# Performance work log

Measured on AMD Instinct MI355X. Metric: run time of the kernel, lower is better.

The kernel has to match this reference:

```python
import jax, jax.numpy as jnp
import numpy as np

DECAY = 0.99
EPS = 1e-05


def setup_inputs() -> dict:
    key = jax.random.key(0)
    k1, k2, k3 = jax.random.split(key, 3)
    N, K, D = 131072, 1024, 64
    return {
        "z": jax.random.normal(k1, (N, D), dtype=jnp.float32),
        "embeddings": jax.random.normal(k2, (K, D), dtype=jnp.float32),
        "cluster_size": jnp.ones((K,), dtype=jnp.float32),
        "ema_embed_sum": jax.random.normal(k3, (K, D), dtype=jnp.float32),
    }


def reference(z, embeddings, cluster_size, ema_embed_sum):
    # z: [N, D]; embeddings/ema_embed_sum: [K, D]; cluster_size: [K]
    N, D = z.shape
    K = embeddings.shape[0]

    # squared pairwise distances via the ||a||^2 - 2ab + ||b||^2 expansion
    d = (
        jnp.sum(z * z, axis=-1, keepdims=True)
        - 2.0 * (z @ embeddings.T)
        + jnp.sum(embeddings * embeddings, axis=-1)
    )  # [N, K]
    encoding_indices = jnp.argmin(d, axis=1)  # [N]
    z_q = embeddings[encoding_indices]  # [N, D]

    # EMA codebook update (training mode; one_hot.sum(0) == counts, one_hot.T @ z == segment_sum)
    counts = jax.ops.segment_sum(jnp.ones((N,), z.dtype), encoding_indices, num_segments=K)
    new_cluster_size = cluster_size * DECAY + (1.0 - DECAY) * counts
    embed_sum = jax.ops.segment_sum(z, encoding_indices, num_segments=K)  # [K, D]
    new_ema_embed_sum = ema_embed_sum * DECAY + (1.0 - DECAY) * embed_sum
    n = jnp.sum(new_cluster_size)
    cs = (new_cluster_size + EPS) / (n + K * EPS) * n
    new_embeddings = new_ema_embed_sum / cs[:, None]

    commitment_loss = jnp.mean((z - z_q) ** 2)
    z_q_st = z + jax.lax.stop_gradient(z_q - z)  # value == z_q
    return (z_q_st, commitment_loss, encoding_indices, new_embeddings, new_cluster_size, new_ema_embed_sum)
```

## Files before the change

kernel.cpp:

```cpp
#include <hip/hip_runtime.h>

#define N_PTS 131072
#define K_CODES 1024
#define DIM 64
#define DECAYF 0.99f
#define OMDF 0.01f
#define EPSF 1e-5f

#define OUT_ZQ      0
#define OUT_LOSS    8388608
#define OUT_IDX     8388609
#define OUT_NEWEMB  8519681
#define OUT_NEWCS   8585217
#define OUT_NEWEMA  8586241

#define WS_C8       0
#define WS_ACNT     8192
#define WS_LOSS     8208
#define WS_EMBSUM   8224
#define WS_ZERO_END 73760
#define WS_ENORM    73760
#define WS_CUR8     74784
#define WS_CS       82976
#define WS_AMBIG    84000
#define WS_ORDER    215072
#define WS_E2       346144

typedef __attribute__((ext_vector_type(8))) short bf16x8;
typedef __attribute__((ext_vector_type(4))) float f32x4;

static __device__ inline short f2bf(float f) {
    unsigned u = __float_as_uint(f);
    unsigned r = (u + 0x7fffu + ((u >> 16) & 1u)) >> 16;
    return (short)r;
}
static __device__ inline float bf2f(short h) {
    return __uint_as_float(((unsigned)(unsigned short)h) << 16);
}

__global__ __launch_bounds__(256) void econv_kernel(const float* __restrict__ E,
                                                    short* __restrict__ E2,
                                                    float* __restrict__ enorm) {
    int k = blockIdx.x * 256 + threadIdx.x;
    const float* ep = E + (size_t)k * DIM;
    short* o = E2 + (size_t)k * 128;
    float s = 0.f;
#pragma unroll
    for (int d = 0; d < 64; ++d) {
        float f = ep[d];
        s += f * f;
        float m = -2.f * f;
        short h = f2bf(m);
        o[d] = h;
        o[64 + d] = f2bf(m - bf2f(h));
    }
    enorm[k] = s;
}

__global__ __launch_bounds__(256) void argmin_mfma(const float* __restrict__ z,
                                                   const short* __restrict__ E2,
                                                   const float* __restrict__ enorm,
                                                   float* __restrict__ out_idx_f,
                                                   float* __restrict__ counts8,
                                                   int* __restrict__ ambig_cnt,
                                                   int* __restrict__ ambig,
                                                   float* __restrict__ loss_ws) {
    int tid = threadIdx.x;
    int w = tid >> 6, lane = tid & 63;
    int c = lane & 15, q = lane >> 4;
    int mbase = blockIdx.x * 256 + w * 64;

    bf16x8 a[4][4];
    float znorm_t[4];
#pragma unroll
    for (int t = 0; t < 4; ++t) {
        const float* zp = z + (size_t)(mbase + t * 16 + c) * DIM;
        const float4* z4a = (const float4*)(zp + q * 8);
        const float4* z4b = (const float4*)(zp + 32 + q * 8);
        float f[16];
        float4 v0 = z4a[0], v1 = z4a[1], v2 = z4b[0], v3 = z4b[1];
        f[0]=v0.x; f[1]=v0.y; f[2]=v0.z; f[3]=v0.w;
        f[4]=v1.x; f[5]=v1.y; f[6]=v1.z; f[7]=v1.w;
        f[8]=v2.x; f[9]=v2.y; f[10]=v2.z; f[11]=v2.w;
        f[12]=v3.x; f[13]=v3.y; f[14]=v3.z; f[15]=v3.w;
        float zn = 0.f;
#pragma unroll
        for (int j = 0; j < 16; ++j) zn += f[j] * f[j];
#pragma unroll
        for (int off = 16; off < 64; off <<= 1) zn += __shfl_xor(zn, off);
        znorm_t[t] = zn;
#pragma unroll
        for (int j = 0; j < 8; ++j) {
            short h0 = f2bf(f[j]);
            a[t][0][j] = h0;
            a[t][2][j] = f2bf(f[j] - bf2f(h0));
            short h1 = f2bf(f[8 + j]);
            a[t][1][j] = h1;
            a[t][3][j] = f2bf(f[8 + j] - bf2f(h1));
        }
    }

    float s1[16], s2[16];
#pragma unroll
    for (int idx = 0; idx < 16; ++idx) { s1[idx] = INFINITY; s2[idx] = INFINITY; }

    unsigned vcode = (unsigned)c;
    for (int tile = 0; tile < 64; ++tile) {
        const bf16x8* bp = (const bf16x8*)E2 + ((size_t)(tile * 16 + c) * 16) + q;
        bf16x8 bh0 = bp[0], bh1 = bp[4], bl0 = bp[8], bl1 = bp[12];
        float en = enorm[tile * 16 + c];
#pragma unroll
        for (int t = 0; t < 4; ++t) {
            f32x4 acc = {en, en, en, en};
            acc = __builtin_amdgcn_mfma_f32_16x16x32_bf16(a[t][0], bl0, acc, 0, 0, 0);
            acc = __builtin_amdgcn_mfma_f32_16x16x32_bf16(a[t][1], bl1, acc, 0, 0, 0);
            acc = __builtin_amdgcn_mfma_f32_16x16x32_bf16(a[t][2], bh0, acc, 0, 0, 0);
            acc = __builtin_amdgcn_mfma_f32_16x16x32_bf16(a[t][3], bh1, acc, 0, 0, 0);
            acc = __builtin_amdgcn_mfma_f32_16x16x32_bf16(a[t][0], bh0, acc, 0, 0, 0);
            acc = __builtin_amdgcn_mfma_f32_16x16x32_bf16(a[t][1], bh1, acc, 0, 0, 0);
#pragma unroll
            for (int i = 0; i < 4; ++i) {
                float sp = __uint_as_float(
                    (__float_as_uint(acc[i]) & 0xFFFFFC00u) | vcode);
                int idx = t * 4 + i;
                float ns2 = __builtin_amdgcn_fmed3f(s1[idx], s2[idx], sp);
                s1[idx] = fminf(s1[idx], sp);
                s2[idx] = ns2;
            }
        }
        vcode += 16;
    }

#pragma unroll
    for (int off = 1; off < 16; off <<= 1) {
#pragma unroll
        for (int idx = 0; idx < 16; ++idx) {
            float os1 = __shfl_xor(s1[idx], off);
            float os2 = __shfl_xor(s2[idx], off);
            float ns1 = fminf(s1[idx], os1);
            s2[idx] = fminf(fmaxf(s1[idx], os1), fminf(s2[idx], os2));
            s1[idx] = ns1;
        }
    }

    float znr[16];
#pragma unroll
    for (int t = 0; t < 4; ++t)
#pragma unroll
        for (int i = 0; i < 4; ++i)
            znr[t * 4 + i] = __shfl(znorm_t[t], (q << 4) | (q * 4 + i), 64);

    __shared__ float lred[16];
    float lsum = 0.f;
    if (c == 0) {
#pragma unroll
        for (int idx = 0; idx < 16; ++idx) {
            int t = idx >> 2, i = idx & 3;
            int row = mbase + t * 16 + q * 4 + i;
            unsigned b1 = __float_as_uint(s1[idx]);
            int code = (int)(b1 & 1023u);
            out_idx_f[row] = (float)code;
            float s1v = __uint_as_float(b1 & 0xFFFFFC00u);
            float gap = s2[idx] - s1[idx];
            float tau = 0.008f + 8e-4f * (fabsf(s1[idx]) + fabsf(s2[idx]));
            if (gap >= tau) {
                atomicAdd(&counts8[(((unsigned)row >> 8) & 7) * K_CODES + code], 1.0f);
                lsum += znr[idx] + s1v;
            } else {
                int p = atomicAdd(ambig_cnt, 1);
                ambig[p] = row;
            }
        }
        lred[w * 4 + q] = lsum;
    }
    __syncthreads();
    if (tid == 0) {
        float tot = 0.f;
#pragma unroll
        for (int i = 0; i < 16; ++i) tot += lred[i];
        atomicAdd(loss_ws, tot);
    }
}

__global__ __launch_bounds__(256) void rescue_kernel(const float* __restrict__ z,
                                                     const float* __restrict__ E,
                                                     const float* __restrict__ enorm,
                                                     const int* __restrict__ ambig_cnt,
                                                     const int* __restrict__ ambig,
                                                     float* __restrict__ out_idx_f,
                                                     float* __restrict__ counts8,
                                                     float* __restrict__ loss_ws) {
    int lane = threadIdx.x & 63;
    int wave = (blockIdx.x * 256 + threadIdx.x) >> 6;
    int nw = gridDim.x * 4;
    int cnt = *ambig_cnt;
    for (int a = 2 * wave; a < cnt; a += 2 * nw) {
        int row0 = ambig[a];
        bool two = (a + 1) < cnt;
        int row1 = two ? ambig[a + 1] : row0;
        const float4* zp0 = (const float4*)(z + (size_t)row0 * DIM);
        const float4* zp1 = (const float4*)(z + (size_t)row1 * DIM);
        float4 zr0[16], zr1[16];
        float zn0 = 0.f, zn1 = 0.f;
#pragma unroll
        for (int i = 0; i < 16; ++i) {
            float4 u = zp0[i], v = zp1[i];
            zr0[i] = u; zr1[i] = v;
            zn0 += u.x * u.x + u.y * u.y + u.z * u.z + u.w * u.w;
            zn1 += v.x * v.x + v.y * v.y + v.z * v.z + v.w * v.w;
        }
        float best0 = INFINITY, best1 = INFINITY;
        int bi0 = 0, bi1 = 0;
        for (int j = 0; j < 16; ++j) {
            int code = j * 64 + lane;
            const float4* ep = (const float4*)(E + (size_t)code * DIM);
            float a0 = 0.f, a1 = 0.f, a2 = 0.f, a3 = 0.f;
            float c0 = 0.f, c1 = 0.f, c2 = 0.f, c3 = 0.f;
#pragma unroll
            for (int i = 0; i < 16; ++i) {
                float4 ev = ep[i];
                a0 += zr0[i].x * ev.x; a1 += zr0[i].y * ev.y;
                a2 += zr0[i].z * ev.z; a3 += zr0[i].w * ev.w;
                c0 += zr1[i].x * ev.x; c1 += zr1[i].y * ev.y;
                c2 += zr1[i].z * ev.z; c3 += zr1[i].w * ev.w;
            }
            float en = enorm[code];
            float s0 = en - 2.f * ((a0 + a1) + (a2 + a3));
            float s1 = en - 2.f * ((c0 + c1) + (c2 + c3));
            if (s0 < best0) { best0 = s0; bi0 = code; }
            if (s1 < best1) { best1 = s1; bi1 = code; }
        }
#pragma unroll
        for (int off = 1; off < 64; off <<= 1) {
            float ob = __shfl_xor(best0, off);
            int oi = __shfl_xor(bi0, off);
            if (ob < best0 || (ob == best0 && oi < bi0)) { best0 = ob; bi0 = oi; }
            float ob1 = __shfl_xor(best1, off);
            int oi1 = __shfl_xor(bi1, off);
            if (ob1 < best1 || (ob1 == best1 && oi1 < bi1)) { best1 = ob1; bi1 = oi1; }
        }
        if (lane == 0) {
            out_idx_f[row0] = (float)bi0;
            atomicAdd(&counts8[(((unsigned)row0 >> 8) & 7) * K_CODES + bi0], 1.0f);
            float ladd = zn0 + best0;
            if (two) {
                out_idx_f[row1] = (float)bi1;
                atomicAdd(&counts8[(((unsigned)row1 >> 8) & 7) * K_CODES + bi1], 1.0f);
                ladd += zn1 + best1;
            }
            atomicAdd(loss_ws, ladd);
        }
    }
}

__global__ __launch_bounds__(256) void zq_write_kernel(const float* __restrict__ E,
                                                       const float* __restrict__ idx_f,
                                                       float* __restrict__ zq) {
    __shared__ int s_k[256];
    int tid = threadIdx.x;
    int rbase = blockIdx.x * 256;
    s_k[tid] = (int)idx_f[rbase + tid];
    __syncthreads();
    size_t ebase = (size_t)rbase * DIM;
#pragma unroll 4
    for (int it = 0; it < 64; ++it) {
        int le = it * 256 + tid;
        int rl = le >> 6, d = le & 63;
        zq[ebase + le] = E[(size_t)s_k[rl] * DIM + d];
    }
}

__global__ __launch_bounds__(1024) void scan_kernel(const float* __restrict__ cluster_size,
                                                    const float* __restrict__ counts8,
                                                    float* __restrict__ ncs_out,
                                                    float* __restrict__ cs_ws,
                                                    int* __restrict__ cursor8) {
    int k = threadIdx.x;
    int lane = k & 63, wv = k >> 6;
    float c8[8];
    float cnt = 0.f;
#pragma unroll
    for (int s = 0; s < 8; ++s) { c8[s] = counts8[s * K_CODES + k]; cnt += c8[s]; }
    float ncs = cluster_size[k] * DECAYF + OMDF * cnt;
    ncs_out[k] = ncs;

    int v = (int)cnt;
    int vs = v;
#pragma unroll
    for (int off = 1; off < 64; off <<= 1) {
        int o = __shfl_up(vs, off, 64);
        if (lane >= off) vs += o;
    }
    float fs = ncs;
#pragma unroll
    for (int off = 1; off < 64; off <<= 1) fs += __shfl_xor(fs, off);

    __shared__ int wtot[16];
    __shared__ float ftot[16];
    __shared__ float nsh;
    if (lane == 63) wtot[wv] = vs;
    if (lane == 0) ftot[wv] = fs;
    __syncthreads();
    if (k == 0) {
        int run = 0; float fn = 0.f;
#pragma unroll
        for (int i = 0; i < 16; ++i) {
            int t = wtot[i]; wtot[i] = run; run += t;
            fn += ftot[i];
        }
        nsh = fn;
    }
    __syncthreads();
    float n = nsh;
    cs_ws[k] = (ncs + EPSF) / (n + (float)K_CODES * EPSF) * n;

    int excl = vs - v + wtot[wv];
    int run = excl;
#pragma unroll
    for (int s = 0; s < 8; ++s) { cursor8[s * K_CODES + k] = run; run += (int)c8[s]; }
}

__global__ __launch_bounds__(256) void scatter_kernel(const float* __restrict__ idx_f,
                                                      int* __restrict__ cursor8,
                                                      int* __restrict__ order) {
    int row = blockIdx.x * 256 + threadIdx.x;
    int k = (int)idx_f[row];
    int shard = ((unsigned)row >> 8) & 7;
    int p = atomicAdd(&cursor8[shard * K_CODES + k], 1);
    order[p] = (k << 17) | row;
}

__global__ __launch_bounds__(256) void segsum_kernel(const float* __restrict__ z,
                                                     const int* __restrict__ order,
                                                     float* __restrict__ embsum) {
    int lane = threadIdx.x & 63;
    int w = threadIdx.x >> 6;
    int wave = blockIdx.x * 4 + w;
    int base = wave * 64;

    int my = order[base + lane];

    int cur = __shfl(my, 0, 64) >> 17;
    float sum = 0.f;
#pragma unroll 8
    for (int i = 0; i < 64; ++i) {
        int p = __shfl(my, i, 64);
        int row = p & 0x1FFFF;
        int code = p >> 17;
        float v = z[(size_t)row * DIM + lane];
        if (code != cur) {
            atomicAdd(&embsum[(size_t)cur * DIM + lane], sum);
            sum = 0.f;
            cur = code;
        }
        sum += v;
    }
    atomicAdd(&embsum[(size_t)cur * DIM + lane], sum);
}

__global__ __launch_bounds__(256) void ema2_kernel(const float* __restrict__ ema,
                                                   const float* __restrict__ embsum,
                                                   const float* __restrict__ cs_ws,
                                                   const float* __restrict__ loss_ws,
                                                   float* __restrict__ newema_out,
                                                   float* __restrict__ newemb_out,
                                                   float* __restrict__ loss_out) {
    int i = blockIdx.x * 256 + threadIdx.x;
    float nes = ema[i] * DECAYF + OMDF * embsum[i];
    newema_out[i] = nes;
    newemb_out[i] = nes / cs_ws[i >> 6];
    if (i == 0)
        loss_out[0] = loss_ws[0] * (1.0f / ((float)N_PTS * (float)DIM));
}

extern "C" void kernel_launch(void* const* d_in, const int* in_sizes, int n_in,
                              void* d_out, int out_size, void* d_ws, size_t ws_size,
                              hipStream_t stream) {
    const float* z            = (const float*)d_in[0];
    const float* E            = (const float*)d_in[1];
    const float* cluster_size = (const float*)d_in[2];
    const float* ema          = (const float*)d_in[3];
    float* out = (float*)d_out;
    float* ws  = (float*)d_ws;

    hipMemsetAsync(ws, 0, (size_t)WS_ZERO_END * sizeof(float), stream);

    econv_kernel<<<4, 256, 0, stream>>>(E, (short*)(ws + WS_E2), ws + WS_ENORM);

    argmin_mfma<<<N_PTS / 256, 256, 0, stream>>>(z, (const short*)(ws + WS_E2),
                                                 ws + WS_ENORM,
                                                 out + OUT_IDX,
                                                 ws + WS_C8,
                                                 (int*)(ws + WS_ACNT),
                                                 (int*)(ws + WS_AMBIG),
                                                 ws + WS_LOSS);

    rescue_kernel<<<512, 256, 0, stream>>>(z, E, ws + WS_ENORM,
                                           (const int*)(ws + WS_ACNT),
                                           (const int*)(ws + WS_AMBIG),
                                           out + OUT_IDX,
                                           ws + WS_C8,
                                           ws + WS_LOSS);

    zq_write_kernel<<<N_PTS / 256, 256, 0, stream>>>(E, out + OUT_IDX,
                                                     out + OUT_ZQ);

    scan_kernel<<<1, 1024, 0, stream>>>(cluster_size, ws + WS_C8,
                                        out + OUT_NEWCS, ws + WS_CS,
                                        (int*)(ws + WS_CUR8));

    scatter_kernel<<<N_PTS / 256, 256, 0, stream>>>(out + OUT_IDX,
                                                    (int*)(ws + WS_CUR8),
                                                    (int*)(ws + WS_ORDER));

    segsum_kernel<<<N_PTS / 256, 256, 0, stream>>>(z,
                                                   (const int*)(ws + WS_ORDER),
                                                   ws + WS_EMBSUM);

    ema2_kernel<<<K_CODES * DIM / 256, 256, 0, stream>>>(ema, ws + WS_EMBSUM,
                                                         ws + WS_CS,
                                                         ws + WS_LOSS,
                                                         out + OUT_NEWEMA,
                                                         out + OUT_NEWEMB,
                                                         out + OUT_LOSS);
}
```

Baseline: 249.0 us.

## Fuse z_q gather into argmin and rescue, shrink argmin tile, fold memset

The separate z_q gather kernel is removed. The argmin kernel now writes z_q rows for confidently assigned points, and the rescue kernel writes them for ambiguous points. The argmin kernel processes 16 rows per wave instead of 64 and launches four times as many blocks with an occupancy hint, trading reuse of each loaded E2 tile for lower register pressure and more waves in flight. The workspace memset is folded into extra blocks of the codebook-conversion kernel, which removes one launch.

```diff
diff --git a/kernel.cpp b/kernel.cpp
--- a/kernel.cpp
+++ b/kernel.cpp
@@ -40,7 +40,14 @@
 
 __global__ __launch_bounds__(256) void econv_kernel(const float* __restrict__ E,
                                                     short* __restrict__ E2,
-                                                    float* __restrict__ enorm) {
+                                                    float* __restrict__ enorm,
+                                                    float* __restrict__ ws0) {
+    if (blockIdx.x >= 4) {
+        for (int i = (blockIdx.x - 4) * 256 + threadIdx.x; i < WS_ZERO_END;
+             i += 32 * 256)
+            ws0[i] = 0.f;
+        return;
+    }
     int k = blockIdx.x * 256 + threadIdx.x;
     const float* ep = E + (size_t)k * DIM;
     short* o = E2 + (size_t)k * 128;
@@ -57,121 +64,119 @@
     enorm[k] = s;
 }
 
-__global__ __launch_bounds__(256) void argmin_mfma(const float* __restrict__ z,
-                                                   const short* __restrict__ E2,
-                                                   const float* __restrict__ enorm,
-                                                   float* __restrict__ out_idx_f,
-                                                   float* __restrict__ counts8,
-                                                   int* __restrict__ ambig_cnt,
-                                                   int* __restrict__ ambig,
-                                                   float* __restrict__ loss_ws) {
+__global__ __launch_bounds__(256, 6) void argmin_mfma(const float* __restrict__ z,
+                                                      const short* __restrict__ E2,
+                                                      const float* __restrict__ enorm,
+                                                      const float* __restrict__ E,
+                                                      float* __restrict__ out_idx_f,
+                                                      float* __restrict__ counts8,
+                                                      int* __restrict__ ambig_cnt,
+                                                      int* __restrict__ ambig,
+                                                      float* __restrict__ loss_ws,
+                                                      float* __restrict__ zq) {
     int tid = threadIdx.x;
     int w = tid >> 6, lane = tid & 63;
     int c = lane & 15, q = lane >> 4;
-    int mbase = blockIdx.x * 256 + w * 64;
-
-    bf16x8 a[4][4];
-    float znorm_t[4];
-#pragma unroll
-    for (int t = 0; t < 4; ++t) {
-        const float* zp = z + (size_t)(mbase + t * 16 + c) * DIM;
-        const float4* z4a = (const float4*)(zp + q * 8);
-        const float4* z4b = (const float4*)(zp + 32 + q * 8);
+    int mbase = blockIdx.x * 64 + w * 16;
+
+    bf16x8 a[4];
+    float zn;
+    {
+        const float* zp = z + (size_t)(mbase + c) * DIM;
+        float4 v0 = *(const float4*)(zp + q * 8);
+        float4 v1 = *(const float4*)(zp + q * 8 + 4);
+        float4 v2 = *(const float4*)(zp + 32 + q * 8);
+        float4 v3 = *(const float4*)(zp + 32 + q * 8 + 4);
         float f[16];
-        float4 v0 = z4a[0], v1 = z4a[1], v2 = z4b[0], v3 = z4b[1];
         f[0]=v0.x; f[1]=v0.y; f[2]=v0.z; f[3]=v0.w;
         f[4]=v1.x; f[5]=v1.y; f[6]=v1.z; f[7]=v1.w;
         f[8]=v2.x; f[9]=v2.y; f[10]=v2.z; f[11]=v2.w;
         f[12]=v3.x; f[13]=v3.y; f[14]=v3.z; f[15]=v3.w;
-        float zn = 0.f;
+        zn = 0.f;
 #pragma unroll
         for (int j = 0; j < 16; ++j) zn += f[j] * f[j];
-#pragma unroll
-        for (int off = 16; off < 64; off <<= 1) zn += __shfl_xor(zn, off);
-        znorm_t[t] = zn;
+        zn += __shfl_xor(zn, 16);
+        zn += __shfl_xor(zn, 32);
 #pragma unroll
         for (int j = 0; j < 8; ++j) {
             short h0 = f2bf(f[j]);
-            a[t][0][j] = h0;
-            a[t][2][j] = f2bf(f[j] - bf2f(h0));
+            a[0][j] = h0;
+            a[2][j] = f2bf(f[j] - bf2f(h0));
             short h1 = f2bf(f[8 + j]);
-            a[t][1][j] = h1;
-            a[t][3][j] = f2bf(f[8 + j] - bf2f(h1));
-        }
-    }
-
-    float s1[16], s2[16];
-#pragma unroll
-    for (int idx = 0; idx < 16; ++idx) { s1[idx] = INFINITY; s2[idx] = INFINITY; }
+            a[1][j] = h1;
+            a[3][j] = f2bf(f[8 + j] - bf2f(h1));
+        }
+    }
+
+    float s1[4] = {INFINITY, INFINITY, INFINITY, INFINITY};
+    float s2[4] = {INFINITY, INFINITY, INFINITY, INFINITY};
 
     unsigned vcode = (unsigned)c;
     for (int tile = 0; tile < 64; ++tile) {
         const bf16x8* bp = (const bf16x8*)E2 + ((size_t)(tile * 16 + c) * 16) + q;
         bf16x8 bh0 = bp[0], bh1 = bp[4], bl0 = bp[8], bl1 = bp[12];
         float en = enorm[tile * 16 + c];
-#pragma unroll
-        for (int t = 0; t < 4; ++t) {
-            f32x4 acc = {en, en, en, en};
-            acc = __builtin_amdgcn_mfma_f32_16x16x32_bf16(a[t][0], bl0, acc, 0, 0, 0);
-            acc = __builtin_amdgcn_mfma_f32_16x16x32_bf16(a[t][1], bl1, acc, 0, 0, 0);
-            acc = __builtin_amdgcn_mfma_f32_16x16x32_bf16(a[t][2], bh0, acc, 0, 0, 0);
-            acc = __builtin_amdgcn_mfma_f32_16x16x32_bf16(a[t][3], bh1, acc, 0, 0, 0);
-            acc = __builtin_amdgcn_mfma_f32_16x16x32_bf16(a[t][0], bh0, acc, 0, 0, 0);
-            acc = __builtin_amdgcn_mfma_f32_16x16x32_bf16(a[t][1], bh1, acc, 0, 0, 0);
+        f32x4 acc = {en, en, en, en};
+        acc = __builtin_amdgcn_mfma_f32_16x16x32_bf16(a[0], bl0, acc, 0, 0, 0);
+        acc = __builtin_amdgcn_mfma_f32_16x16x32_bf16(a[1], bl1, acc, 0, 0, 0);
+        acc = __builtin_amdgcn_mfma_f32_16x16x32_bf16(a[2], bh0, acc, 0, 0, 0);
+        acc = __builtin_amdgcn_mfma_f32_16x16x32_bf16(a[3], bh1, acc, 0, 0, 0);
+        acc = __builtin_amdgcn_mfma_f32_16x16x32_bf16(a[0], bh0, acc, 0, 0, 0);
+        acc = __builtin_amdgcn_mfma_f32_16x16x32_bf16(a[1], bh1, acc, 0, 0, 0);
+#pragma unroll
+        for (int i = 0; i < 4; ++i) {
+            float sp = __uint_as_float(
+                (__float_as_uint(acc[i]) & 0xFFFFFC00u) | vcode);
+            float ns2 = __builtin_amdgcn_fmed3f(s1[i], s2[i], sp);
+            s1[i] = fminf(s1[i], sp);
+            s2[i] = ns2;
+        }
+        vcode += 16;
+    }
+
+#pragma unroll
+    for (int off = 1; off < 16; off <<= 1) {
+#pragma unroll
+        for (int i = 0; i < 4; ++i) {
+            float os1 = __shfl_xor(s1[i], off);
+            float os2 = __shfl_xor(s2[i], off);
+            float ns1 = fminf(s1[i], os1);
+            s2[i] = fminf(fmaxf(s1[i], os1), fminf(s2[i], os2));
+            s1[i] = ns1;
+        }
+    }
+
+    float znr[4];
+#pragma unroll
+    for (int i = 0; i < 4; ++i) znr[i] = __shfl(zn, q * 4 + i);
+
+    __shared__ float lred[16];
+    int code_s[4], flag_s[4];
+    {
+        float lsum = 0.f;
+        if (c == 0) {
 #pragma unroll
             for (int i = 0; i < 4; ++i) {
-                float sp = __uint_as_float(
-                    (__float_as_uint(acc[i]) & 0xFFFFFC00u) | vcode);
-                int idx = t * 4 + i;
-                float ns2 = __builtin_amdgcn_fmed3f(s1[idx], s2[idx], sp);
-                s1[idx] = fminf(s1[idx], sp);
-                s2[idx] = ns2;
+                int row = mbase + q * 4 + i;
+                unsigned b1 = __float_as_uint(s1[i]);
+                int code = (int)(b1 & 1023u);
+                code_s[i] = code;
+                out_idx_f[row] = (float)code;
+                float s1v = __uint_as_float(b1 & 0xFFFFFC00u);
+                float gap = s2[i] - s1[i];
+                float tau = 0.008f + 8e-4f * (fabsf(s1[i]) + fabsf(s2[i]));
+                if (gap >= tau) {
+                    flag_s[i] = 1;
+                    atomicAdd(&counts8[(((unsigned)row >> 8) & 7) * K_CODES + code], 1.0f);
+                    lsum += znr[i] + s1v;
+                } else {
+                    flag_s[i] = 0;
+                    int p = atomicAdd(ambig_cnt, 1);
+                    ambig[p] = row;
+                }
             }
-        }
-        vcode += 16;
-    }
-
-#pragma unroll
-    for (int off = 1; off < 16; off <<= 1) {
-#pragma unroll
-        for (int idx = 0; idx < 16; ++idx) {
-            float os1 = __shfl_xor(s1[idx], off);
-            float os2 = __shfl_xor(s2[idx], off);
-            float ns1 = fminf(s1[idx], os1);
-            s2[idx] = fminf(fmaxf(s1[idx], os1), fminf(s2[idx], os2));
-            s1[idx] = ns1;
-        }
-    }
-
-    float znr[16];
-#pragma unroll
-    for (int t = 0; t < 4; ++t)
-#pragma unroll
-        for (int i = 0; i < 4; ++i)
-            znr[t * 4 + i] = __shfl(znorm_t[t], (q << 4) | (q * 4 + i), 64);
-
-    __shared__ float lred[16];
-    float lsum = 0.f;
-    if (c == 0) {
-#pragma unroll
-        for (int idx = 0; idx < 16; ++idx) {
-            int t = idx >> 2, i = idx & 3;
-            int row = mbase + t * 16 + q * 4 + i;
-            unsigned b1 = __float_as_uint(s1[idx]);
-            int code = (int)(b1 & 1023u);
-            out_idx_f[row] = (float)code;
-            float s1v = __uint_as_float(b1 & 0xFFFFFC00u);
-            float gap = s2[idx] - s1[idx];
-            float tau = 0.008f + 8e-4f * (fabsf(s1[idx]) + fabsf(s2[idx]));
-            if (gap >= tau) {
-                atomicAdd(&counts8[(((unsigned)row >> 8) & 7) * K_CODES + code], 1.0f);
-                lsum += znr[idx] + s1v;
-            } else {
-                int p = atomicAdd(ambig_cnt, 1);
-                ambig[p] = row;
-            }
-        }
-        lred[w * 4 + q] = lsum;
+            lred[w * 4 + q] = lsum;
+        }
     }
     __syncthreads();
     if (tid == 0) {
@@ -179,6 +184,15 @@
 #pragma unroll
         for (int i = 0; i < 16; ++i) tot += lred[i];
         atomicAdd(loss_ws, tot);
+    }
+
+#pragma unroll
+    for (int r = 0; r < 16; ++r) {
+        int holder = (r >> 2) << 4;
+        int code = __shfl(code_s[r & 3], holder);
+        int fl   = __shfl(flag_s[r & 3], holder);
+        if (fl)
+            zq[(size_t)(mbase + r) * DIM + lane] = E[(size_t)code * DIM + lane];
     }
 }
 
@@ -189,7 +203,8 @@
                                                      const int* __restrict__ ambig,
                                                      float* __restrict__ out_idx_f,
                                                      float* __restrict__ counts8,
-                                                     float* __restrict__ loss_ws) {
+                                                     float* __restrict__ loss_ws,
+                                                     float* __restrict__ zq) {
     int lane = threadIdx.x & 63;
     int wave = (blockIdx.x * 256 + threadIdx.x) >> 6;
     int nw = gridDim.x * 4;
@@ -239,6 +254,8 @@
             int oi1 = __shfl_xor(bi1, off);
             if (ob1 < best1 || (ob1 == best1 && oi1 < bi1)) { best1 = ob1; bi1 = oi1; }
         }
+        zq[(size_t)row0 * DIM + lane] = E[(size_t)bi0 * DIM + lane];
+        if (two) zq[(size_t)row1 * DIM + lane] = E[(size_t)bi1 * DIM + lane];
         if (lane == 0) {
             out_idx_f[row0] = (float)bi0;
             atomicAdd(&counts8[(((unsigned)row0 >> 8) & 7) * K_CODES + bi0], 1.0f);
@@ -250,23 +267,6 @@
             }
             atomicAdd(loss_ws, ladd);
         }
-    }
-}
-
-__global__ __launch_bounds__(256) void zq_write_kernel(const float* __restrict__ E,
-                                                       const float* __restrict__ idx_f,
-                                                       float* __restrict__ zq) {
-    __shared__ int s_k[256];
-    int tid = threadIdx.x;
-    int rbase = blockIdx.x * 256;
-    s_k[tid] = (int)idx_f[rbase + tid];
-    __syncthreads();
-    size_t ebase = (size_t)rbase * DIM;
-#pragma unroll 4
-    for (int it = 0; it < 64; ++it) {
-        int le = it * 256 + tid;
-        int rl = le >> 6, d = le & 63;
-        zq[ebase + le] = E[(size_t)s_k[rl] * DIM + d];
     }
 }
 
@@ -383,27 +383,25 @@
     float* out = (float*)d_out;
     float* ws  = (float*)d_ws;
 
-    hipMemsetAsync(ws, 0, (size_t)WS_ZERO_END * sizeof(float), stream);
-
-    econv_kernel<<<4, 256, 0, stream>>>(E, (short*)(ws + WS_E2), ws + WS_ENORM);
-
-    argmin_mfma<<<N_PTS / 256, 256, 0, stream>>>(z, (const short*)(ws + WS_E2),
-                                                 ws + WS_ENORM,
-                                                 out + OUT_IDX,
-                                                 ws + WS_C8,
-                                                 (int*)(ws + WS_ACNT),
-                                                 (int*)(ws + WS_AMBIG),
-                                                 ws + WS_LOSS);
+    econv_kernel<<<36, 256, 0, stream>>>(E, (short*)(ws + WS_E2),
+                                         ws + WS_ENORM, ws);
+
+    argmin_mfma<<<N_PTS / 64, 256, 0, stream>>>(z, (const short*)(ws + WS_E2),
+                                                ws + WS_ENORM, E,
+                                                out + OUT_IDX,
+                                                ws + WS_C8,
+                                                (int*)(ws + WS_ACNT),
+                                                (int*)(ws + WS_AMBIG),
+                                                ws + WS_LOSS,
+                                                out + OUT_ZQ);
 
     rescue_kernel<<<512, 256, 0, stream>>>(z, E, ws + WS_ENORM,
                                            (const int*)(ws + WS_ACNT),
                                            (const int*)(ws + WS_AMBIG),
                                            out + OUT_IDX,
                                            ws + WS_C8,
-                                           ws + WS_LOSS);
-
-    zq_write_kernel<<<N_PTS / 256, 256, 0, stream>>>(E, out + OUT_IDX,
-                                                     out + OUT_ZQ);
+                                           ws + WS_LOSS,
+                                           out + OUT_ZQ);
 
     scan_kernel<<<1, 1024, 0, stream>>>(cluster_size, ws + WS_C8,
                                         out + OUT_NEWCS, ws + WS_CS,
```

Result: slower. 432.0 us (+73.5%).

## Fuse rescue and z_q gather into argmin, replace sort-based segsum with LDS histogram

Applied to the files above, without the earlier changes.

Ambiguous rows are now re-checked exactly inside the argmin block, using a per-block shared-memory list, and the same block writes z_q rows. This removes the separate rescue and z_q write kernels. The scan/scatter/segment-sum pipeline is replaced by one kernel that builds per-block shared-memory partial sums of z per code (16-dim slices) and flushes them with global atomics, and one extra block computes cluster sizes. The workspace memset is folded into extra blocks of the conversion kernel. The risk is that rescue work now runs serially per block with only 4 waves, and the shared-memory float atomics may contend.

```diff
diff --git a/kernel.cpp b/kernel.cpp
--- a/kernel.cpp
+++ b/kernel.cpp
@@ -15,16 +15,12 @@
 #define OUT_NEWEMA  8586241
 
 #define WS_C8       0
-#define WS_ACNT     8192
-#define WS_LOSS     8208
-#define WS_EMBSUM   8224
-#define WS_ZERO_END 73760
-#define WS_ENORM    73760
-#define WS_CUR8     74784
-#define WS_CS       82976
-#define WS_AMBIG    84000
-#define WS_ORDER    215072
-#define WS_E2       346144
+#define WS_LOSS     8192
+#define WS_EMBSUM   8208
+#define WS_ZERO_END 73744
+#define WS_ENORM    73744
+#define WS_CS       74768
+#define WS_E2       75792
 
 typedef __attribute__((ext_vector_type(8))) short bf16x8;
 typedef __attribute__((ext_vector_type(4))) float f32x4;
@@ -40,7 +36,14 @@
 
 __global__ __launch_bounds__(256) void econv_kernel(const float* __restrict__ E,
                                                     short* __restrict__ E2,
-                                                    float* __restrict__ enorm) {
+                                                    float* __restrict__ enorm,
+                                                    float* __restrict__ ws0) {
+    if (blockIdx.x >= 4) {
+        for (int i = (blockIdx.x - 4) * 256 + threadIdx.x; i < WS_ZERO_END;
+             i += 32 * 256)
+            ws0[i] = 0.f;
+        return;
+    }
     int k = blockIdx.x * 256 + threadIdx.x;
     const float* ep = E + (size_t)k * DIM;
     short* o = E2 + (size_t)k * 128;
@@ -60,15 +63,24 @@
 __global__ __launch_bounds__(256) void argmin_mfma(const float* __restrict__ z,
                                                    const short* __restrict__ E2,
                                                    const float* __restrict__ enorm,
+                                                   const float* __restrict__ E,
                                                    float* __restrict__ out_idx_f,
                                                    float* __restrict__ counts8,
-                                                   int* __restrict__ ambig_cnt,
-                                                   int* __restrict__ ambig,
-                                                   float* __restrict__ loss_ws) {
+                                                   float* __restrict__ loss_ws,
+                                                   float* __restrict__ zq) {
+    __shared__ int s_info[256];
+    __shared__ int s_alist[256];
+    __shared__ int s_acnt;
+    __shared__ float lred[16];
+
     int tid = threadIdx.x;
     int w = tid >> 6, lane = tid & 63;
     int c = lane & 15, q = lane >> 4;
-    int mbase = blockIdx.x * 256 + w * 64;
+    int rbase = blockIdx.x * 256;
+    int mbase = rbase + w * 64;
+
+    if (tid == 0) s_acnt = 0;
+    __syncthreads();
 
     bf16x8 a[4][4];
     float znorm_t[4];
@@ -150,212 +162,154 @@
         for (int i = 0; i < 4; ++i)
             znr[t * 4 + i] = __shfl(znorm_t[t], (q << 4) | (q * 4 + i), 64);
 
-    __shared__ float lred[16];
-    float lsum = 0.f;
-    if (c == 0) {
-#pragma unroll
-        for (int idx = 0; idx < 16; ++idx) {
-            int t = idx >> 2, i = idx & 3;
-            int row = mbase + t * 16 + q * 4 + i;
-            unsigned b1 = __float_as_uint(s1[idx]);
-            int code = (int)(b1 & 1023u);
-            out_idx_f[row] = (float)code;
-            float s1v = __uint_as_float(b1 & 0xFFFFFC00u);
-            float gap = s2[idx] - s1[idx];
-            float tau = 0.008f + 8e-4f * (fabsf(s1[idx]) + fabsf(s2[idx]));
-            if (gap >= tau) {
-                atomicAdd(&counts8[(((unsigned)row >> 8) & 7) * K_CODES + code], 1.0f);
-                lsum += znr[idx] + s1v;
-            } else {
-                int p = atomicAdd(ambig_cnt, 1);
-                ambig[p] = row;
+    {
+        float lsum = 0.f;
+        if (c == 0) {
+#pragma unroll
+            for (int idx = 0; idx < 16; ++idx) {
+                int t = idx >> 2, i = idx & 3;
+                int rib = w * 64 + t * 16 + q * 4 + i;
+                int row = rbase + rib;
+                unsigned b1 = __float_as_uint(s1[idx]);
+                int code = (int)(b1 & 1023u);
+                float s1v = __uint_as_float(b1 & 0xFFFFFC00u);
+                float gap = s2[idx] - s1[idx];
+                float tau = 0.008f + 8e-4f * (fabsf(s1[idx]) + fabsf(s2[idx]));
+                if (gap >= tau) {
+                    s_info[rib] = code;
+                    out_idx_f[row] = (float)code;
+                    atomicAdd(&counts8[(((unsigned)row >> 8) & 7) * K_CODES + code], 1.0f);
+                    lsum += znr[idx] + s1v;
+                } else {
+                    s_info[rib] = code | 1024;
+                    int p = atomicAdd(&s_acnt, 1);
+                    s_alist[p] = rib;
+                }
             }
-        }
-        lred[w * 4 + q] = lsum;
+            lred[w * 4 + q] = lsum;
+        }
     }
     __syncthreads();
+
     if (tid == 0) {
         float tot = 0.f;
 #pragma unroll
         for (int i = 0; i < 16; ++i) tot += lred[i];
         atomicAdd(loss_ws, tot);
     }
-}
-
-__global__ __launch_bounds__(256) void rescue_kernel(const float* __restrict__ z,
-                                                     const float* __restrict__ E,
-                                                     const float* __restrict__ enorm,
-                                                     const int* __restrict__ ambig_cnt,
-                                                     const int* __restrict__ ambig,
-                                                     float* __restrict__ out_idx_f,
-                                                     float* __restrict__ counts8,
-                                                     float* __restrict__ loss_ws) {
-    int lane = threadIdx.x & 63;
-    int wave = (blockIdx.x * 256 + threadIdx.x) >> 6;
-    int nw = gridDim.x * 4;
-    int cnt = *ambig_cnt;
-    for (int a = 2 * wave; a < cnt; a += 2 * nw) {
-        int row0 = ambig[a];
-        bool two = (a + 1) < cnt;
-        int row1 = two ? ambig[a + 1] : row0;
-        const float4* zp0 = (const float4*)(z + (size_t)row0 * DIM);
-        const float4* zp1 = (const float4*)(z + (size_t)row1 * DIM);
-        float4 zr0[16], zr1[16];
-        float zn0 = 0.f, zn1 = 0.f;
+
+    for (int it = 0; it < 64; ++it) {
+        int le = it * 256 + tid;
+        int rl = le >> 6, d = le & 63;
+        int info = s_info[rl];
+        if (!(info & 1024))
+            zq[(size_t)(rbase + rl) * DIM + d] = E[(size_t)(info & 1023) * DIM + d];
+    }
+
+    int acnt = s_acnt;
+    for (int aI = w; aI < acnt; aI += 4) {
+        int rib = s_alist[aI];
+        int row = rbase + rib;
+        const float4* zp = (const float4*)(z + (size_t)row * DIM);
+        float4 zr[16];
+        float zn2 = 0.f;
 #pragma unroll
         for (int i = 0; i < 16; ++i) {
-            float4 u = zp0[i], v = zp1[i];
-            zr0[i] = u; zr1[i] = v;
-            zn0 += u.x * u.x + u.y * u.y + u.z * u.z + u.w * u.w;
-            zn1 += v.x * v.x + v.y * v.y + v.z * v.z + v.w * v.w;
-        }
-        float best0 = INFINITY, best1 = INFINITY;
-        int bi0 = 0, bi1 = 0;
+            float4 u = zp[i];
+            zr[i] = u;
+            zn2 += u.x * u.x + u.y * u.y + u.z * u.z + u.w * u.w;
+        }
+        float best = INFINITY;
+        int bi = 0;
         for (int j = 0; j < 16; ++j) {
             int code = j * 64 + lane;
             const float4* ep = (const float4*)(E + (size_t)code * DIM);
             float a0 = 0.f, a1 = 0.f, a2 = 0.f, a3 = 0.f;
-            float c0 = 0.f, c1 = 0.f, c2 = 0.f, c3 = 0.f;
 #pragma unroll
             for (int i = 0; i < 16; ++i) {
                 float4 ev = ep[i];
-                a0 += zr0[i].x * ev.x; a1 += zr0[i].y * ev.y;
-                a2 += zr0[i].z * ev.z; a3 += zr0[i].w * ev.w;
-                c0 += zr1[i].x * ev.x; c1 += zr1[i].y * ev.y;
-                c2 += zr1[i].z * ev.z; c3 += zr1[i].w * ev.w;
+                a0 += zr[i].x * ev.x; a1 += zr[i].y * ev.y;
+                a2 += zr[i].z * ev.z; a3 += zr[i].w * ev.w;
             }
-            float en = enorm[code];
-            float s0 = en - 2.f * ((a0 + a1) + (a2 + a3));
-            float s1 = en - 2.f * ((c0 + c1) + (c2 + c3));
-            if (s0 < best0) { best0 = s0; bi0 = code; }
-            if (s1 < best1) { best1 = s1; bi1 = code; }
+            float s = enorm[code] - 2.f * ((a0 + a1) + (a2 + a3));
+            if (s < best) { best = s; bi = code; }
         }
 #pragma unroll
         for (int off = 1; off < 64; off <<= 1) {
-            float ob = __shfl_xor(best0, off);
-            int oi = __shfl_xor(bi0, off);
-            if (ob < best0 || (ob == best0 && oi < bi0)) { best0 = ob; bi0 = oi; }
-            float ob1 = __shfl_xor(best1, off);
-            int oi1 = __shfl_xor(bi1, off);
-            if (ob1 < best1 || (ob1 == best1 && oi1 < bi1)) { best1 = ob1; bi1 = oi1; }
-        }
+            float ob = __shfl_xor(best, off);
+            int oi = __shfl_xor(bi, off);
+            if (ob < best || (ob == best && oi < bi)) { best = ob; bi = oi; }
+        }
+        zq[(size_t)row * DIM + lane] = E[(size_t)bi * DIM + lane];
         if (lane == 0) {
-            out_idx_f[row0] = (float)bi0;
-            atomicAdd(&counts8[(((unsigned)row0 >> 8) & 7) * K_CODES + bi0], 1.0f);
-            float ladd = zn0 + best0;
-            if (two) {
-                out_idx_f[row1] = (float)bi1;
-                atomicAdd(&counts8[(((unsigned)row1 >> 8) & 7) * K_CODES + bi1], 1.0f);
-                ladd += zn1 + best1;
-            }
-            atomicAdd(loss_ws, ladd);
-        }
-    }
-}
-
-__global__ __launch_bounds__(256) void zq_write_kernel(const float* __restrict__ E,
-                                                       const float* __restrict__ idx_f,
-                                                       float* __restrict__ zq) {
-    __shared__ int s_k[256];
+            out_idx_f[row] = (float)bi;
+            atomicAdd(&counts8[(((unsigned)row >> 8) & 7) * K_CODES + bi], 1.0f);
+            atomicAdd(loss_ws, zn2 + best);
+        }
+    }
+}
+
+__global__ __launch_bounds__(256) void histsum_kernel(const float* __restrict__ z,
+                                                      const float* __restrict__ idx_f,
+                                                      const float* __restrict__ cluster_size,
+                                                      const float* __restrict__ counts8,
+                                                      float* __restrict__ embsum,
+                                                      float* __restrict__ ncs_out,
+                                                      float* __restrict__ cs_ws) {
+    __shared__ float hist[K_CODES * 16];
     int tid = threadIdx.x;
-    int rbase = blockIdx.x * 256;
-    s_k[tid] = (int)idx_f[rbase + tid];
+
+    if (blockIdx.x == 128) {
+        float ncs_r[4];
+        float part = 0.f;
+#pragma unroll
+        for (int j = 0; j < 4; ++j) {
+            int k = tid * 4 + j;
+            float cnt = 0.f;
+#pragma unroll
+            for (int s = 0; s < 8; ++s) cnt += counts8[s * K_CODES + k];
+            float ncs = cluster_size[k] * DECAYF + OMDF * cnt;
+            ncs_out[k] = ncs;
+            ncs_r[j] = ncs;
+            part += ncs;
+        }
+#pragma unroll
+        for (int off = 1; off < 64; off <<= 1) part += __shfl_xor(part, off);
+        if ((tid & 63) == 0) hist[tid >> 6] = part;
+        __syncthreads();
+        float n = hist[0] + hist[1] + hist[2] + hist[3];
+#pragma unroll
+        for (int j = 0; j < 4; ++j) {
+            int k = tid * 4 + j;
+            cs_ws[k] = (ncs_r[j] + EPSF) / (n + (float)K_CODES * EPSF) * n;
+        }
+        return;
+    }
+
+    int slice = blockIdx.x & 3;
+    int rbase = (blockIdx.x >> 2) * 4096;
+
+    for (int i = tid; i < K_CODES * 16; i += 256) hist[i] = 0.f;
     __syncthreads();
-    size_t ebase = (size_t)rbase * DIM;
-#pragma unroll 4
+
+    int dl = (tid & 3) * 4;
     for (int it = 0; it < 64; ++it) {
-        int le = it * 256 + tid;
-        int rl = le >> 6, d = le & 63;
-        zq[ebase + le] = E[(size_t)s_k[rl] * DIM + d];
-    }
-}
-
-__global__ __launch_bounds__(1024) void scan_kernel(const float* __restrict__ cluster_size,
-                                                    const float* __restrict__ counts8,
-                                                    float* __restrict__ ncs_out,
-                                                    float* __restrict__ cs_ws,
-                                                    int* __restrict__ cursor8) {
-    int k = threadIdx.x;
-    int lane = k & 63, wv = k >> 6;
-    float c8[8];
-    float cnt = 0.f;
-#pragma unroll
-    for (int s = 0; s < 8; ++s) { c8[s] = counts8[s * K_CODES + k]; cnt += c8[s]; }
-    float ncs = cluster_size[k] * DECAYF + OMDF * cnt;
-    ncs_out[k] = ncs;
-
-    int v = (int)cnt;
-    int vs = v;
-#pragma unroll
-    for (int off = 1; off < 64; off <<= 1) {
-        int o = __shfl_up(vs, off, 64);
-        if (lane >= off) vs += o;
-    }
-    float fs = ncs;
-#pragma unroll
-    for (int off = 1; off < 64; off <<= 1) fs += __shfl_xor(fs, off);
-
-    __shared__ int wtot[16];
-    __shared__ float ftot[16];
-    __shared__ float nsh;
-    if (lane == 63) wtot[wv] = vs;
-    if (lane == 0) ftot[wv] = fs;
+        int row = rbase + it * 64 + (tid >> 2);
+        int code = (int)idx_f[row];
+        float4 v = *(const float4*)(z + (size_t)row * DIM + slice * 16 + dl);
+        float* h = &hist[code * 16 + dl];
+        atomicAdd(&h[0], v.x);
+        atomicAdd(&h[1], v.y);
+        atomicAdd(&h[2], v.z);
+        atomicAdd(&h[3], v.w);
+    }
     __syncthreads();
-    if (k == 0) {
-        int run = 0; float fn = 0.f;
-#pragma unroll
-        for (int i = 0; i < 16; ++i) {
-            int t = wtot[i]; wtot[i] = run; run += t;
-            fn += ftot[i];
-        }
-        nsh = fn;
-    }
-    __syncthreads();
-    float n = nsh;
-    cs_ws[k] = (ncs + EPSF) / (n + (float)K_CODES * EPSF) * n;
-
-    int excl = vs - v + wtot[wv];
-    int run = excl;
-#pragma unroll
-    for (int s = 0; s < 8; ++s) { cursor8[s * K_CODES + k] = run; run += (int)c8[s]; }
-}
-
-__global__ __launch_bounds__(256) void scatter_kernel(const float* __restrict__ idx_f,
-                                                      int* __restrict__ cursor8,
-                                                      int* __restrict__ order) {
-    int row = blockIdx.x * 256 + threadIdx.x;
-    int k = (int)idx_f[row];
-    int shard = ((unsigned)row >> 8) & 7;
-    int p = atomicAdd(&cursor8[shard * K_CODES + k], 1);
-    order[p] = (k << 17) | row;
-}
-
-__global__ __launch_bounds__(256) void segsum_kernel(const float* __restrict__ z,
-                                                     const int* __restrict__ order,
-                                                     float* __restrict__ embsum) {
-    int lane = threadIdx.x & 63;
-    int w = threadIdx.x >> 6;
-    int wave = blockIdx.x * 4 + w;
-    int base = wave * 64;
-
-    int my = order[base + lane];
-
-    int cur = __shfl(my, 0, 64) >> 17;
-    float sum = 0.f;
-#pragma unroll 8
-    for (int i = 0; i < 64; ++i) {
-        int p = __shfl(my, i, 64);
-        int row = p & 0x1FFFF;
-        int code = p >> 17;
-        float v = z[(size_t)row * DIM + lane];
-        if (code != cur) {
-            atomicAdd(&embsum[(size_t)cur * DIM + lane], sum);
-            sum = 0.f;
-            cur = code;
-        }
-        sum += v;
-    }
-    atomicAdd(&embsum[(size_t)cur * DIM + lane], sum);
+
+    for (int i = tid; i < K_CODES * 16; i += 256) {
+        float v = hist[i];
+        if (v != 0.f)
+            atomicAdd(&embsum[(size_t)(i >> 4) * DIM + slice * 16 + (i & 15)], v);
+    }
 }
 
 __global__ __launch_bounds__(256) void ema2_kernel(const float* __restrict__ ema,
@@ -383,39 +337,21 @@
     float* out = (float*)d_out;
     float* ws  = (float*)d_ws;
 
-    hipMemsetAsync(ws, 0, (size_t)WS_ZERO_END * sizeof(float), stream);
-
-    econv_kernel<<<4, 256, 0, stream>>>(E, (short*)(ws + WS_E2), ws + WS_ENORM);
+    econv_kernel<<<36, 256, 0, stream>>>(E, (short*)(ws + WS_E2),
+                                         ws + WS_ENORM, ws);
 
     argmin_mfma<<<N_PTS / 256, 256, 0, stream>>>(z, (const short*)(ws + WS_E2),
-                                                 ws + WS_ENORM,
+                                                 ws + WS_ENORM, E,
                                                  out + OUT_IDX,
                                                  ws + WS_C8,
-                                                 (int*)(ws + WS_ACNT),
-                                                 (int*)(ws + WS_AMBIG),
-                                                 ws + WS_LOSS);
-
-    rescue_kernel<<<512, 256, 0, stream>>>(z, E, ws + WS_ENORM,
-                                           (const int*)(ws + WS_ACNT),
-                                           (const int*)(ws + WS_AMBIG),
-                                           out + OUT_IDX,
-                                           ws + WS_C8,
-                                           ws + WS_LOSS);
-
-    zq_write_kernel<<<N_PTS / 256, 256, 0, stream>>>(E, out + OUT_IDX,
-                                                     out + OUT_ZQ);
-
-    scan_kernel<<<1, 1024, 0, stream>>>(cluster_size, ws + WS_C8,
-                                        out + OUT_NEWCS, ws + WS_CS,
-                                        (int*)(ws + WS_CUR8));
-
-    scatter_kernel<<<N_PTS / 256, 256, 0, stream>>>(out + OUT_IDX,
-                                                    (int*)(ws + WS_CUR8),
-                                                    (int*)(ws + WS_ORDER));
-
-    segsum_kernel<<<N_PTS / 256, 256, 0, stream>>>(z,
-                                                   (const int*)(ws + WS_ORDER),
-                                                   ws + WS_EMBSUM);
+                                                 ws + WS_LOSS,
+                                                 out + OUT_ZQ);
+
+    histsum_kernel<<<129, 256, 0, stream>>>(z, out + OUT_IDX, cluster_size,
+                                            ws + WS_C8,
+                                            ws + WS_EMBSUM,
+                                            out + OUT_NEWCS,
+                                            ws + WS_CS);
 
     ema2_kernel<<<K_CODES * DIM / 256, 256, 0, stream>>>(ema, ws + WS_EMBSUM,
                                                          ws + WS_CS,
```

Measured after the change: 351.8 us. 41.3% more time.
